# Optimization experiments

Measured on AMD Instinct MI355X. Metric: run time of the kernel, lower is better.

The kernel has to match this reference:

```python
import jax, jax.numpy as jnp
import numpy as np

D = 1024      # model_size
H = 16        # n_heads
HD = D // H   # head_size
B = 8
S = 1024


def setup_inputs() -> dict:
    key = jax.random.key(0)
    ks = jax.random.split(key, 8)
    sq = lambda k, shp: jax.random.normal(k, shp, dtype=jnp.float32) * (1.0 / np.sqrt(shp[0]))
    return {
        "query": jax.random.normal(ks[0], (B, S, D), dtype=jnp.float32),
        "value": jax.random.normal(ks[1], (B, S, D), dtype=jnp.float32),
        "Wq": sq(ks[2], (D, D)),
        "bq": jnp.zeros((D,), dtype=jnp.float32),
        "Wkv": sq(ks[3], (D, 2 * D)),
        "bkv": jnp.zeros((2 * D,), dtype=jnp.float32),
        "Wo": sq(ks[4], (D, D)),
        "bo": jnp.zeros((D,), dtype=jnp.float32),
    }


def reference(query, value, Wq, bq, Wkv, bkv, Wo, bo):
    scale = 1.0 / jnp.sqrt(jnp.float32(HD))
    q = query @ Wq + bq                      # [B,S,D]
    kv = value @ Wkv + bkv                   # [B,S,2D]
    # tf.split(kv, 2H): chunks 0..H-1 are K heads, H..2H-1 are V heads
    k = kv[..., :D].reshape(B, S, H, HD)
    v = kv[..., D:].reshape(B, S, H, HD)
    qh = q.reshape(B, S, H, HD)
    scores = jnp.einsum("bqhd,bkhd->bhqk", qh, k) * scale   # [B,H,S,S]
    attn = jax.nn.softmax(scores, axis=-1)
    heads = jnp.einsum("bhqk,bkhd->bqhd", attn, v).reshape(B, S, D)
    return heads @ Wo + bo
```

## Files before the change

kernel.cpp:

```cpp
#include <hip/hip_runtime.h>
#include <math.h>

#define B_  8
#define S_  1024
#define D_  1024
#define H_  16
#define HD_ 64

typedef float          floatx4  __attribute__((ext_vector_type(4)));
typedef __bf16         bf16x8   __attribute__((ext_vector_type(8)));
typedef unsigned int   uintx2   __attribute__((ext_vector_type(2)));
typedef unsigned int   uintx4   __attribute__((ext_vector_type(4)));

__device__ __forceinline__ unsigned short f2bf(float f) {
    union { float f; unsigned u; } v; v.f = f;
    unsigned r = v.u + 0x7FFFu + ((v.u >> 16) & 1u);
    return (unsigned short)(r >> 16);
}
__device__ __forceinline__ unsigned pk2(float a, float b) {
    union { __bf16 h[2]; unsigned u; } r;
    r.h[0] = (__bf16)a; r.h[1] = (__bf16)b;
    return r.u;
}
__device__ __forceinline__ void async16(const void* g, void* l) {
    __builtin_amdgcn_global_load_lds(
        (__attribute__((address_space(1))) void*)g,
        (__attribute__((address_space(3))) void*)l, 16, 0, 0);
}

__global__ __launch_bounds__(256) void prep_k(const float* __restrict__ query,
                                              const float* __restrict__ value,
                                              unsigned short* __restrict__ qbf,
                                              unsigned short* __restrict__ vbf,
                                              const float* __restrict__ Wq,
                                              const float* __restrict__ Wkv,
                                              const float* __restrict__ Wo,
                                              unsigned short* __restrict__ WqT,
                                              unsigned short* __restrict__ WkvT,
                                              unsigned short* __restrict__ WoT) {
    __shared__ float T[64 * 68];
    const int t   = threadIdx.x;
    const int bid = blockIdx.x;
    if (bid < 8192) {
        int i = bid * 256 + t;
        floatx4 a = ((const floatx4*)query)[i];
        floatx4 b = ((const floatx4*)value)[i];
        uintx2 oa = { pk2(a[0], a[1]), pk2(a[2], a[3]) };
        uintx2 ob = { pk2(b[0], b[1]), pk2(b[2], b[3]) };
        ((uintx2*)qbf)[i] = oa;
        ((uintx2*)vbf)[i] = ob;
        return;
    }
    const int lin = bid - 8192;
    const int z   = lin >> 8;
    const float* W; unsigned short* WT; int Ndim, nbase;
    if (z == 0)      { W = Wq;  WT = WqT;  Ndim = 1024; nbase = 0; }
    else if (z == 3) { W = Wo;  WT = WoT;  Ndim = 1024; nbase = 0; }
    else             { W = Wkv; WT = WkvT; Ndim = 2048; nbase = (z - 1) * 1024; }
    const int n0 = (lin & 15) * 64 + nbase;
    const int k0 = ((lin >> 4) & 15) * 64;
#pragma unroll
    for (int rep = 0; rep < 4; ++rep) {
        int kl = (t >> 4) + rep * 16;
        int ns = (t & 15) * 4;
        *(floatx4*)(T + kl * 68 + ns) = *(const floatx4*)(W + (size_t)(k0 + kl) * Ndim + n0 + ns);
    }
    __syncthreads();
#pragma unroll
    for (int rep = 0; rep < 2; ++rep) {
        int nl = (t >> 3) + rep * 32;
        int ks = (t & 7) * 8;
        union { unsigned short s[8]; uintx4 u; } o;
#pragma unroll
        for (int j = 0; j < 8; ++j) o.s[j] = f2bf(T[(ks + j) * 68 + nl]);
        *(uintx4*)(WT + (size_t)(n0 + nl) * 1024 + k0 + ks) = o.u;
    }
}

template<int SWAP>
__device__ __forceinline__ void kloop(const unsigned short* __restrict__ ga0,
                                      const unsigned short* __restrict__ gb0,
                                      unsigned short* __restrict__ As,
                                      unsigned short* __restrict__ Bs,
                                      floatx4 (&acc)[4][4],
                                      int w, int lane) {
    const int quad = lane >> 4;
    const int l15  = lane & 15;
    const int e7   = l15 & 7;
    const int wr   = (w >> 1) * 64;
    const int wc   = (w & 1) * 64;
    for (int k0 = 0; k0 < 1024; k0 += 64) {
        if (k0) __syncthreads();
#pragma unroll
        for (int i = 0; i < 4; ++i) {
            int c = i * 4 + w;
            async16(ga0 + (size_t)(c * 8) * 1024 + k0, As + c * 512);
            async16(gb0 + (size_t)(c * 8) * 1024 + k0, Bs + c * 512);
        }
        __syncthreads();
#pragma unroll
        for (int ks = 0; ks < 2; ++ks) {
            bf16x8 af[4], bf[4];
#pragma unroll
            for (int mi = 0; mi < 4; ++mi)
                af[mi] = *(const bf16x8*)(As + (wr + mi * 16 + l15) * 64 + (((ks * 4 + quad) ^ e7) * 8));
#pragma unroll
            for (int ni = 0; ni < 4; ++ni)
                bf[ni] = *(const bf16x8*)(Bs + (wc + ni * 16 + l15) * 64 + (((ks * 4 + quad) ^ e7) * 8));
#pragma unroll
            for (int mi = 0; mi < 4; ++mi)
#pragma unroll
                for (int ni = 0; ni < 4; ++ni)
                    acc[mi][ni] = SWAP
                        ? __builtin_amdgcn_mfma_f32_16x16x32_bf16(bf[ni], af[mi], acc[mi][ni], 0, 0, 0)
                        : __builtin_amdgcn_mfma_f32_16x16x32_bf16(af[mi], bf[ni], acc[mi][ni], 0, 0, 0);
        }
    }
}

__global__ __launch_bounds__(256, 4) void qkv_gemm_k(const unsigned short* __restrict__ qbf,
                                                     const unsigned short* __restrict__ vbf,
                                                     const unsigned short* __restrict__ WqT,
                                                     const unsigned short* __restrict__ WkvT,
                                                     const float* __restrict__ bq,
                                                     const float* __restrict__ bkv,
                                                     unsigned short* __restrict__ Qb,
                                                     unsigned short* __restrict__ Kb,
                                                     unsigned short* __restrict__ Vtg,
                                                     float cexp) {
    __shared__ unsigned short As[128 * 64];
    __shared__ unsigned short Bs[128 * 64];
    const int t    = threadIdx.x;
    const int lane = t & 63;
    const int w    = t >> 6;
    const int quad = lane >> 4;
    const int l15  = lane & 15;
    const int wr   = (w >> 1) * 64;
    const int wc   = (w & 1) * 64;
    const int lrow = lane >> 3;
    const int lswz = ((lane & 7) ^ lrow) * 8;

    const int bid = blockIdx.x;
    int m0, n0;
    const unsigned short *Ap, *Wp;
    const float* bp;
    unsigned short* outp;
    float sc;
    bool vpath = false;
    if (bid < 512) {
        m0 = (bid & 63) * 128; n0 = (bid >> 6) * 128;
        Ap = qbf; Wp = WqT; bp = bq; outp = Qb; sc = cexp;
    } else {
        int b2 = bid - 512;
        m0 = (b2 & 63) * 128; n0 = (b2 >> 6) * 128;
        Ap = vbf; Wp = WkvT; bp = bkv; outp = Kb; sc = 1.0f;
        vpath = (n0 >= 1024);
    }

    floatx4 acc[4][4] = {};
    const unsigned short* ga0 = Ap + (size_t)(m0 + lrow) * 1024 + lswz;
    const unsigned short* gb0 = Wp + (size_t)(n0 + lrow) * 1024 + lswz;

    if (!vpath) {
        kloop<1>(ga0, gb0, As, Bs, acc, w, lane);
#pragma unroll
        for (int ni = 0; ni < 4; ++ni) {
            const int nb = n0 + wc + ni * 16 + quad * 4;
            const floatx4 b4 = *(const floatx4*)(bp + nb);
#pragma unroll
            for (int mi = 0; mi < 4; ++mi) {
                const int m = m0 + wr + mi * 16 + l15;
                floatx4 v = acc[mi][ni];
                uintx2 o = { pk2((v[0] + b4[0]) * sc, (v[1] + b4[1]) * sc),
                             pk2((v[2] + b4[2]) * sc, (v[3] + b4[3]) * sc) };
                *(uintx2*)(outp + (size_t)m * 1024 + (nb & 1023)) = o;
            }
        }
    } else {
        kloop<0>(ga0, gb0, As, Bs, acc, w, lane);
        const int bb = m0 >> 10;
#pragma unroll
        for (int ni = 0; ni < 4; ++ni) {
            const int n = n0 + wc + ni * 16 + l15;
            const int c = n - 1024;
            const float bv = bp[n];
#pragma unroll
            for (int mi = 0; mi < 4; ++mi) {
                const int m = m0 + wr + mi * 16 + quad * 4;
                const int s = m & 1023;
                floatx4 v = acc[mi][ni];
                uintx2 o = { pk2(v[0] + bv, v[1] + bv), pk2(v[2] + bv, v[3] + bv) };
                *(uintx2*)(Vtg + ((size_t)(bb * 1024 + c)) * 1024 + s) = o;
            }
        }
    }
}

__global__ __launch_bounds__(256, 4) void o_gemm_k(const unsigned short* __restrict__ Hb,
                                                   const unsigned short* __restrict__ WoT,
                                                   const float* __restrict__ bo,
                                                   float* __restrict__ out) {
    __shared__ unsigned short As[128 * 64];
    __shared__ unsigned short Bs[128 * 64];
    const int t    = threadIdx.x;
    const int lane = t & 63;
    const int w    = t >> 6;
    const int quad = lane >> 4;
    const int l15  = lane & 15;
    const int wr   = (w >> 1) * 64;
    const int wc   = (w & 1) * 64;
    const int lrow = lane >> 3;
    const int lswz = ((lane & 7) ^ lrow) * 8;
    const int m0   = (blockIdx.x & 63) * 128;
    const int n0   = (blockIdx.x >> 6) * 128;

    floatx4 acc[4][4] = {};
    const unsigned short* ga0 = Hb  + (size_t)(m0 + lrow) * 1024 + lswz;
    const unsigned short* gb0 = WoT + (size_t)(n0 + lrow) * 1024 + lswz;
    kloop<1>(ga0, gb0, As, Bs, acc, w, lane);

#pragma unroll
    for (int ni = 0; ni < 4; ++ni) {
        const int nb = n0 + wc + ni * 16 + quad * 4;
        const floatx4 b4 = *(const floatx4*)(bo + nb);
#pragma unroll
        for (int mi = 0; mi < 4; ++mi) {
            const int m = m0 + wr + mi * 16 + l15;
            floatx4 v = acc[mi][ni];
            floatx4 o = { v[0] + b4[0], v[1] + b4[1], v[2] + b4[2], v[3] + b4[3] };
            *(floatx4*)(out + (size_t)m * 1024 + nb) = o;
        }
    }
}

__global__ __launch_bounds__(256) void attn_kernel(const unsigned short* __restrict__ Qb,
                                                   const unsigned short* __restrict__ Kb,
                                                   const unsigned short* __restrict__ Vtg,
                                                   unsigned short* __restrict__ Hb) {
    __shared__ unsigned short QPs[128 * 64];
    __shared__ unsigned short Ks[64 * 64];
    __shared__ unsigned short Vs[64 * 64];

    const int lin = blockIdx.x;
    const int xcd = lin & 7;
    const int grp = lin >> 3;
    const int bh  = xcd * 16 + (grp >> 3);
    const int qt  = grp & 7;
    const int b   = bh >> 4;
    const int h   = bh & 15;
    const int q0  = qt * 128;

    const int t    = threadIdx.x;
    const int lane = t & 63;
    const int w    = t >> 6;
    const int quad = lane >> 4;
    const int l15  = lane & 15;
    const int e7   = l15 & 7;
    const int lrow = lane >> 3;
    const int lswz = ((lane & 7) ^ lrow) * 8;

    {
        const unsigned short* gq = Qb + ((size_t)(b * S_ + q0)) * D_ + h * HD_;
#pragma unroll
        for (int i = 0; i < 4; ++i) {
            int r0 = (w * 4 + i) * 8;
            async16(gq + (size_t)(r0 + lrow) * D_ + lswz, QPs + r0 * 64);
        }
    }
    __syncthreads();

    bf16x8 bQ[2][2];
#pragma unroll
    for (int ks = 0; ks < 2; ++ks)
#pragma unroll
        for (int ni = 0; ni < 2; ++ni)
            bQ[ks][ni] = *(const bf16x8*)(QPs + (w * 32 + ni * 16 + l15) * 64 + ((ks * 4 + quad) ^ e7) * 8);

    const unsigned short* gkbase = Kb  + ((size_t)b * S_) * D_ + h * HD_;
    const unsigned short* gvbase = Vtg + ((size_t)(b * D_ + h * HD_)) * S_;

    float   lsum[2] = { 0.f, 0.f };
    floatx4 oacc[4][2] = {};
    unsigned short* Psw = QPs + w * (32 * 64);

    for (int k0 = 0; k0 < S_; k0 += 64) {
        __syncthreads();
#pragma unroll
        for (int j = 0; j < 2; ++j) {
            int r0 = (w * 2 + j) * 8;
            async16(gkbase + (size_t)(k0 + r0 + lrow) * D_ + lswz, Ks + r0 * 64);
            async16(gvbase + (size_t)(r0 + lrow) * S_ + k0 + lswz, Vs + r0 * 64);
        }
        __syncthreads();

        floatx4 st[4][2] = {};
#pragma unroll
        for (int ks = 0; ks < 2; ++ks) {
            bf16x8 aK[4];
#pragma unroll
            for (int mi = 0; mi < 4; ++mi)
                aK[mi] = *(const bf16x8*)(Ks + (mi * 16 + l15) * 64 + ((ks * 4 + quad) ^ e7) * 8);
#pragma unroll
            for (int mi = 0; mi < 4; ++mi)
#pragma unroll
                for (int ni = 0; ni < 2; ++ni)
                    st[mi][ni] = __builtin_amdgcn_mfma_f32_16x16x32_bf16(aK[mi], bQ[ks][ni], st[mi][ni], 0, 0, 0);
        }

#pragma unroll
        for (int ni = 0; ni < 2; ++ni) {
            float ls = 0.f;
#pragma unroll
            for (int mi = 0; mi < 4; ++mi) {
                float p0 = __builtin_amdgcn_exp2f(st[mi][ni][0]);
                float p1 = __builtin_amdgcn_exp2f(st[mi][ni][1]);
                float p2 = __builtin_amdgcn_exp2f(st[mi][ni][2]);
                float p3 = __builtin_amdgcn_exp2f(st[mi][ni][3]);
                ls += (p0 + p1) + (p2 + p3);
                uintx2 pk = { pk2(p0, p1), pk2(p2, p3) };
                *(uintx2*)(Psw + (ni * 16 + l15) * 64 +
                           (((2 * mi + (quad >> 1)) ^ e7) * 8 + (quad & 1) * 4)) = pk;
            }
            lsum[ni] += ls;
        }

#pragma unroll
        for (int ks = 0; ks < 2; ++ks) {
            bf16x8 aV[4], bP[2];
#pragma unroll
            for (int mi = 0; mi < 4; ++mi)
                aV[mi] = *(const bf16x8*)(Vs + (mi * 16 + l15) * 64 + ((ks * 4 + quad) ^ e7) * 8);
#pragma unroll
            for (int ni = 0; ni < 2; ++ni)
                bP[ni] = *(const bf16x8*)(Psw + (ni * 16 + l15) * 64 + ((ks * 4 + quad) ^ e7) * 8);
#pragma unroll
            for (int mi = 0; mi < 4; ++mi)
#pragma unroll
                for (int ni = 0; ni < 2; ++ni)
                    oacc[mi][ni] = __builtin_amdgcn_mfma_f32_16x16x32_bf16(aV[mi], bP[ni], oacc[mi][ni], 0, 0, 0);
        }
    }

    float rl[2];
#pragma unroll
    for (int ni = 0; ni < 2; ++ni) {
        float l = lsum[ni];
        l += __shfl_xor(l, 16);
        l += __shfl_xor(l, 32);
        rl[ni] = 1.f / l;
    }
#pragma unroll
    for (int mi = 0; mi < 4; ++mi)
#pragma unroll
        for (int ni = 0; ni < 2; ++ni) {
            uintx2 pk = { pk2(oacc[mi][ni][0] * rl[ni], oacc[mi][ni][1] * rl[ni]),
                          pk2(oacc[mi][ni][2] * rl[ni], oacc[mi][ni][3] * rl[ni]) };
            *(uintx2*)(Psw + (ni * 16 + l15) * 64 +
                       (((2 * mi + (quad >> 1)) ^ e7) * 8 + (quad & 1) * 4)) = pk;
        }
    {
        int qrow = lane >> 1;
        int kh   = lane & 1;
        size_t obase = ((size_t)(b * S_ + q0 + w * 32 + qrow)) * D_ + h * HD_ + kh * 32;
        int e = qrow & 7;
#pragma unroll
        for (int j = 0; j < 4; ++j) {
            int chunk = kh * 4 + j;
            *(uintx4*)(Hb + obase + j * 8) =
                *(const uintx4*)(Psw + qrow * 64 + ((chunk ^ e) * 8));
        }
    }
}

extern "C" void kernel_launch(void* const* d_in, const int* in_sizes, int n_in,
                              void* d_out, int out_size, void* d_ws, size_t ws_size,
                              hipStream_t stream) {
    (void)in_sizes; (void)n_in; (void)out_size; (void)ws_size;
    const float* query = (const float*)d_in[0];
    const float* value = (const float*)d_in[1];
    const float* Wq    = (const float*)d_in[2];
    const float* bq    = (const float*)d_in[3];
    const float* Wkv   = (const float*)d_in[4];
    const float* bkv   = (const float*)d_in[5];
    const float* Wo    = (const float*)d_in[6];
    const float* bo    = (const float*)d_in[7];

    const size_t MS = (size_t)B_ * S_;
    char* p = (char*)d_ws;
    unsigned short* qbf  = (unsigned short*)p; p += MS * D_ * 2;
    unsigned short* vbf  = (unsigned short*)p; p += MS * D_ * 2;
    unsigned short* WqT  = (unsigned short*)p; p += (size_t)D_ * D_ * 2;
    unsigned short* WkvT = (unsigned short*)p; p += (size_t)2 * D_ * D_ * 2;
    unsigned short* WoT  = (unsigned short*)p; p += (size_t)D_ * D_ * 2;
    unsigned short* Qb   = (unsigned short*)p; p += MS * D_ * 2;
    unsigned short* Kb   = (unsigned short*)p; p += MS * D_ * 2;
    unsigned short* Vtg  = (unsigned short*)p; p += MS * D_ * 2;
    unsigned short* Hb   = qbf;

    const float cexp = 0.125f * 1.44269504088896341f;

    prep_k<<<9216, 256, 0, stream>>>(query, value, qbf, vbf, Wq, Wkv, Wo, WqT, WkvT, WoT);
    qkv_gemm_k<<<1536, 256, 0, stream>>>(qbf, vbf, WqT, WkvT, bq, bkv, Qb, Kb, Vtg, cexp);
    attn_kernel<<<1024, 256, 0, stream>>>(Qb, Kb, Vtg, Hb);
    o_gemm_k<<<512, 256, 0, stream>>>(Hb, WoT, bo, (float*)d_out);
}
```

Before: 268.6 us.

## Double-buffer attention K/V tiles, shrink O-GEMM tile, use packed bf16 convert

The attention kernel now double-buffers K and V in shared memory and prefetches the next 64-key tile while computing on the current one. This removes one barrier per iteration and hides global-load latency, at the cost of doubling K/V LDS usage. The output projection GEMM moves from 128x128 to 128x64 tiles with an inlined k-loop and twice as many blocks, trading operand reuse for more parallelism. pk2 uses the hardware packed bf16 convert builtin when it is available.

```diff
diff --git a/kernel.cpp b/kernel.cpp
--- a/kernel.cpp
+++ b/kernel.cpp
@@ -18,9 +18,15 @@
     return (unsigned short)(r >> 16);
 }
 __device__ __forceinline__ unsigned pk2(float a, float b) {
+#if __has_builtin(__builtin_amdgcn_cvt_pk_bf16_f32)
+    union { __bf16 h[2]; unsigned u; } r;
+    *(__attribute__((ext_vector_type(2))) __bf16*)&r = __builtin_amdgcn_cvt_pk_bf16_f32(a, b);
+    return r.u;
+#else
     union { __bf16 h[2]; unsigned u; } r;
     r.h[0] = (__bf16)a; r.h[1] = (__bf16)b;
     return r.u;
+#endif
 }
 __device__ __forceinline__ void async16(const void* g, void* l) {
     __builtin_amdgcn_global_load_lds(
@@ -201,26 +207,56 @@
                                                    const float* __restrict__ bo,
                                                    float* __restrict__ out) {
     __shared__ unsigned short As[128 * 64];
-    __shared__ unsigned short Bs[128 * 64];
+    __shared__ unsigned short Bs[64 * 64];
     const int t    = threadIdx.x;
     const int lane = t & 63;
     const int w    = t >> 6;
     const int quad = lane >> 4;
     const int l15  = lane & 15;
+    const int e7   = l15 & 7;
     const int wr   = (w >> 1) * 64;
-    const int wc   = (w & 1) * 64;
+    const int wc   = (w & 1) * 32;
     const int lrow = lane >> 3;
     const int lswz = ((lane & 7) ^ lrow) * 8;
     const int m0   = (blockIdx.x & 63) * 128;
-    const int n0   = (blockIdx.x >> 6) * 128;
-
-    floatx4 acc[4][4] = {};
+    const int n0   = (blockIdx.x >> 6) * 64;
+
+    floatx4 acc[4][2] = {};
     const unsigned short* ga0 = Hb  + (size_t)(m0 + lrow) * 1024 + lswz;
     const unsigned short* gb0 = WoT + (size_t)(n0 + lrow) * 1024 + lswz;
-    kloop<1>(ga0, gb0, As, Bs, acc, w, lane);
-
-#pragma unroll
-    for (int ni = 0; ni < 4; ++ni) {
+
+    for (int k0 = 0; k0 < 1024; k0 += 64) {
+        if (k0) __syncthreads();
+#pragma unroll
+        for (int i = 0; i < 4; ++i) {
+            int c = i * 4 + w;
+            async16(ga0 + (size_t)(c * 8) * 1024 + k0, As + c * 512);
+        }
+#pragma unroll
+        for (int i = 0; i < 2; ++i) {
+            int c = i * 4 + w;
+            async16(gb0 + (size_t)(c * 8) * 1024 + k0, Bs + c * 512);
+        }
+        __syncthreads();
+#pragma unroll
+        for (int ks = 0; ks < 2; ++ks) {
+            bf16x8 af[4], bf[2];
+#pragma unroll
+            for (int mi = 0; mi < 4; ++mi)
+                af[mi] = *(const bf16x8*)(As + (wr + mi * 16 + l15) * 64 + (((ks * 4 + quad) ^ e7) * 8));
+#pragma unroll
+            for (int ni = 0; ni < 2; ++ni)
+                bf[ni] = *(const bf16x8*)(Bs + (wc + ni * 16 + l15) * 64 + (((ks * 4 + quad) ^ e7) * 8));
+#pragma unroll
+            for (int mi = 0; mi < 4; ++mi)
+#pragma unroll
+                for (int ni = 0; ni < 2; ++ni)
+                    acc[mi][ni] = __builtin_amdgcn_mfma_f32_16x16x32_bf16(bf[ni], af[mi], acc[mi][ni], 0, 0, 0);
+        }
+    }
+
+#pragma unroll
+    for (int ni = 0; ni < 2; ++ni) {
         const int nb = n0 + wc + ni * 16 + quad * 4;
         const floatx4 b4 = *(const floatx4*)(bo + nb);
 #pragma unroll
@@ -238,8 +274,8 @@
                                                    const unsigned short* __restrict__ Vtg,
                                                    unsigned short* __restrict__ Hb) {
     __shared__ unsigned short QPs[128 * 64];
-    __shared__ unsigned short Ks[64 * 64];
-    __shared__ unsigned short Vs[64 * 64];
+    __shared__ unsigned short Ks[2][64 * 64];
+    __shared__ unsigned short Vs[2][64 * 64];
 
     const int lin = blockIdx.x;
     const int xcd = lin & 7;
@@ -259,6 +295,9 @@
     const int lrow = lane >> 3;
     const int lswz = ((lane & 7) ^ lrow) * 8;
 
+    const unsigned short* gkbase = Kb  + ((size_t)b * S_) * D_ + h * HD_;
+    const unsigned short* gvbase = Vtg + ((size_t)(b * D_ + h * HD_)) * S_;
+
     {
         const unsigned short* gq = Qb + ((size_t)(b * S_ + q0)) * D_ + h * HD_;
 #pragma unroll
@@ -266,6 +305,12 @@
             int r0 = (w * 4 + i) * 8;
             async16(gq + (size_t)(r0 + lrow) * D_ + lswz, QPs + r0 * 64);
         }
+#pragma unroll
+        for (int j = 0; j < 2; ++j) {
+            int r0 = (w * 2 + j) * 8;
+            async16(gkbase + (size_t)(r0 + lrow) * D_ + lswz, Ks[0] + r0 * 64);
+            async16(gvbase + (size_t)(r0 + lrow) * S_ + lswz, Vs[0] + r0 * 64);
+        }
     }
     __syncthreads();
 
@@ -275,23 +320,25 @@
 #pragma unroll
         for (int ni = 0; ni < 2; ++ni)
             bQ[ks][ni] = *(const bf16x8*)(QPs + (w * 32 + ni * 16 + l15) * 64 + ((ks * 4 + quad) ^ e7) * 8);
-
-    const unsigned short* gkbase = Kb  + ((size_t)b * S_) * D_ + h * HD_;
-    const unsigned short* gvbase = Vtg + ((size_t)(b * D_ + h * HD_)) * S_;
 
     float   lsum[2] = { 0.f, 0.f };
     floatx4 oacc[4][2] = {};
     unsigned short* Psw = QPs + w * (32 * 64);
 
-    for (int k0 = 0; k0 < S_; k0 += 64) {
+    for (int it = 0; it < 16; ++it) {
+        const int cur = it & 1;
         __syncthreads();
-#pragma unroll
-        for (int j = 0; j < 2; ++j) {
-            int r0 = (w * 2 + j) * 8;
-            async16(gkbase + (size_t)(k0 + r0 + lrow) * D_ + lswz, Ks + r0 * 64);
-            async16(gvbase + (size_t)(r0 + lrow) * S_ + k0 + lswz, Vs + r0 * 64);
-        }
-        __syncthreads();
+        if (it < 15) {
+            const int k0n = (it + 1) * 64;
+#pragma unroll
+            for (int j = 0; j < 2; ++j) {
+                int r0 = (w * 2 + j) * 8;
+                async16(gkbase + (size_t)(k0n + r0 + lrow) * D_ + lswz, Ks[cur ^ 1] + r0 * 64);
+                async16(gvbase + (size_t)(r0 + lrow) * S_ + k0n + lswz, Vs[cur ^ 1] + r0 * 64);
+            }
+        }
+        const unsigned short* Kc = Ks[cur];
+        const unsigned short* Vc = Vs[cur];
 
         floatx4 st[4][2] = {};
 #pragma unroll
@@ -299,7 +346,7 @@
             bf16x8 aK[4];
 #pragma unroll
             for (int mi = 0; mi < 4; ++mi)
-                aK[mi] = *(const bf16x8*)(Ks + (mi * 16 + l15) * 64 + ((ks * 4 + quad) ^ e7) * 8);
+                aK[mi] = *(const bf16x8*)(Kc + (mi * 16 + l15) * 64 + ((ks * 4 + quad) ^ e7) * 8);
 #pragma unroll
             for (int mi = 0; mi < 4; ++mi)
 #pragma unroll
@@ -329,7 +376,7 @@
             bf16x8 aV[4], bP[2];
 #pragma unroll
             for (int mi = 0; mi < 4; ++mi)
-                aV[mi] = *(const bf16x8*)(Vs + (mi * 16 + l15) * 64 + ((ks * 4 + quad) ^ e7) * 8);
+                aV[mi] = *(const bf16x8*)(Vc + (mi * 16 + l15) * 64 + ((ks * 4 + quad) ^ e7) * 8);
 #pragma unroll
             for (int ni = 0; ni < 2; ++ni)
                 bP[ni] = *(const bf16x8*)(Psw + (ni * 16 + l15) * 64 + ((ks * 4 + quad) ^ e7) * 8);
@@ -402,5 +449,5 @@
     prep_k<<<9216, 256, 0, stream>>>(query, value, qbf, vbf, Wq, Wkv, Wo, WqT, WkvT, WoT);
     qkv_gemm_k<<<1536, 256, 0, stream>>>(qbf, vbf, WqT, WkvT, bq, bkv, Qb, Kb, Vtg, cexp);
     attn_kernel<<<1024, 256, 0, stream>>>(Qb, Kb, Vtg, Hb);
-    o_gemm_k<<<512, 256, 0, stream>>>(Hb, WoT, bo, (float*)d_out);
-}
+    o_gemm_k<<<1024, 256, 0, stream>>>(Hb, WoT, bo, (float*)d_out);
+}
```

After: 281.5 us. 4.8% more time.
